# Kernel tuning notes

Measured on AMD Instinct MI355X. Metric: run time of the kernel, lower is better.

The kernel has to match this reference:

```python
import jax, jax.numpy as jnp
import numpy as np

# Model dims (match init_kwargs)
D_MODEL = 768
D_STATE = 128
HEADDIM = 64
EXPAND = 2
D_CONV = 4
D_INNER = EXPAND * D_MODEL              # 1536 (== d_ssm)
NHEADS = D_INNER // HEADDIM             # 24
CONV_DIM = D_INNER + 2 * D_STATE        # 1792
D_IN_PROJ = 2 * D_INNER + 2 * D_STATE + NHEADS  # 3352
BATCH, SEQLEN = 2, 512


def setup_inputs() -> dict:
    key = jax.random.key(0)
    ks = jax.random.split(key, 8)
    u = jax.random.normal(ks[0], (BATCH, SEQLEN, D_MODEL), jnp.float32)
    W_in = jax.random.normal(ks[1], (D_IN_PROJ, D_MODEL), jnp.float32) * 0.02
    conv_w = jax.random.normal(ks[2], (CONV_DIM, D_CONV), jnp.float32) * 0.3
    conv_b = jax.random.normal(ks[3], (CONV_DIM,), jnp.float32) * 0.1
    # dt_bias = inverse-softplus of dt sampled log-uniform in [dt_min, dt_max]
    dt = jnp.exp(jax.random.uniform(ks[4], (NHEADS,)) * (np.log(0.02) - np.log(1e-3)) + np.log(1e-3))
    dt_bias = dt + jnp.log(-jnp.expm1(-dt))
    A_log = jnp.log(jax.random.uniform(ks[5], (NHEADS,), minval=1.0, maxval=16.0))
    D_param = jnp.ones((NHEADS,), jnp.float32)
    W_out = jax.random.normal(ks[6], (D_MODEL, D_INNER), jnp.float32) * 0.02
    return dict(u=u, W_in=W_in, conv_w=conv_w, conv_b=conv_b,
                dt_bias=dt_bias, A_log=A_log, D_param=D_param, W_out=W_out)


def _mamba2_scan(u, W_in, conv_w, conv_b, dt_bias, A_log, D_param, W_out):
    B, L, _ = u.shape
    A = -jnp.exp(A_log)  # (H,)

    def step(carry, u_t):
        conv_state, ssm_state = carry  # (B, CONV_DIM, D_CONV), (B, H, P, N)
        zxbcdt = u_t @ W_in.T          # (B, D_IN_PROJ); d_mlp == 0
        z = zxbcdt[:, :D_INNER]
        xBC = zxbcdt[:, D_INNER:D_INNER + CONV_DIM]
        dt = zxbcdt[:, D_INNER + CONV_DIM:]
        # causal depthwise conv state update (roll + write last)
        conv_state = jnp.concatenate([conv_state[:, :, 1:], xBC[:, :, None]], axis=-1)
        xbc = jax.nn.silu(jnp.sum(conv_state * conv_w[None], axis=-1) + conv_b)
        x = xbc[:, :D_INNER]
        Bm = xbc[:, D_INNER:D_INNER + D_STATE]
        Cm = xbc[:, D_INNER + D_STATE:]
        dt = jax.nn.softplus(dt + dt_bias)          # (B, H)
        dA = jnp.exp(dt * A)                        # (B, H)
        xh = x.reshape(B, NHEADS, HEADDIM)          # (B, H, P)
        dBx = jnp.einsum('bh,bn,bhp->bhpn', dt, Bm, xh)
        ssm_state = ssm_state * dA[:, :, None, None] + dBx
        y = jnp.einsum('bhpn,bn->bhp', ssm_state, Cm) + D_param[None, :, None] * xh
        y = y.reshape(B, D_INNER) * jax.nn.silu(z)  # gate (rmsnorm=False)
        return (conv_state, ssm_state), y @ W_out.T

    init = (jnp.zeros((B, CONV_DIM, D_CONV), u.dtype),
            jnp.zeros((B, NHEADS, HEADDIM, D_STATE), u.dtype))
    _, ys = jax.lax.scan(jax.checkpoint(step), init, jnp.swapaxes(u, 0, 1))
    return jnp.swapaxes(ys, 0, 1)  # (B, L, D_MODEL)


def reference(u, W_in, conv_w, conv_b, dt_bias, A_log, D_param, W_out):
    return _mamba2_scan(u, W_in, conv_w, conv_b, dt_bias, A_log, D_param, W_out)
```

## Files before the change

kernel.cpp:

```cpp
#include <hip/hip_runtime.h>
#include <math.h>

#define B_     2
#define L_     512
#define DM     768
#define DS     128
#define HD     64
#define DI     1536
#define NH     24
#define CONVD  1792
#define DPROJ  3352
#define ML     (B_*L_)
#define Q      64
#define NC     (L_/Q)
#define NPAD1  3456

typedef __bf16 bf16x8 __attribute__((ext_vector_type(8)));
typedef float f32x4 __attribute__((ext_vector_type(4)));

__device__ __forceinline__ float sigmoidf_(float x){ return 1.f/(1.f+__expf(-x)); }
__device__ __forceinline__ ushort bf16rn(float x){
  uint u = __float_as_uint(x);
  u += 0x7fff + ((u>>16)&1);
  return (ushort)(u>>16);
}
__device__ __forceinline__ float bf2f(ushort h){ return __uint_as_float(((uint)h)<<16); }
__device__ __forceinline__ void gll16(const void* g, void* l){
  __builtin_amdgcn_global_load_lds((const __attribute__((address_space(1))) void*)g,
                                   (__attribute__((address_space(3))) void*)l, 16, 0, 0);
}

__device__ __forceinline__ void cvt4(const float* srcp, ushort* dsth, ushort* dstl, bool valid){
  float4 v = valid ? *(const float4*)srcp : make_float4(0,0,0,0);
  float xv[4] = {v.x,v.y,v.z,v.w};
  ushort h[4], l[4];
#pragma unroll
  for (int j=0;j<4;j++){ h[j]=bf16rn(xv[j]); l[j]=bf16rn(xv[j]-bf2f(h[j])); }
  *(uint2*)dsth = make_uint2((uint)h[0]|((uint)h[1]<<16), (uint)h[2]|((uint)h[3]<<16));
  *(uint2*)dstl = make_uint2((uint)l[0]|((uint)l[1]<<16), (uint)l[2]|((uint)l[3]<<16));
}

__launch_bounds__(256)
__global__ void cvt_all(const float* __restrict__ u, const float* __restrict__ W_in,
                        const float* __restrict__ W_out,
                        ushort* __restrict__ uS, ushort* __restrict__ WinS,
                        ushort* __restrict__ WoutS, float* __restrict__ out, int outN4){
  const int N1 = ML*(DM/4);
  const int N2 = NPAD1*(DM/4);
  const int N3 = DM*(DI/4);
  int idx = blockIdx.x*256 + threadIdx.x;
  if (idx < N1){
    int r = idx/(DM/4), c = (idx - r*(DM/4))<<2;
    cvt4(&u[(size_t)r*DM + c], &uS[(size_t)r*2*DM + c], &uS[(size_t)r*2*DM + DM + c], true);
  } else if (idx < N1+N2){
    int li = idx - N1;
    int r = li/(DM/4), c = (li - r*(DM/4))<<2;
    bool valid = r < DPROJ;
    cvt4(&W_in[(size_t)(valid ? r : 0)*DM + c], &WinS[(size_t)r*2*DM + c], &WinS[(size_t)r*2*DM + DM + c], valid);
  } else if (idx < N1+N2+N3){
    int li = idx - N1 - N2;
    int r = li/(DI/4), c = (li - r*(DI/4))<<2;
    cvt4(&W_out[(size_t)r*DI + c], &WoutS[(size_t)r*2*DI + c], &WoutS[(size_t)r*2*DI + DI + c], true);
  } else {
    int o = idx - (N1+N2+N3);
    if (o < outN4) *(float4*)&out[(size_t)o*4] = make_float4(0,0,0,0);
  }
}

template<int BM,int BN,int K,int SPLITK,bool ATOMIC>
__launch_bounds__(256, 2)
__global__ void gemm4(const ushort* __restrict__ AS, const ushort* __restrict__ BS,
                      float* __restrict__ C, int Nvalid, int Nstore){
  constexpr int KS = K / SPLITK;
  constexpr int STEPS = KS / 64;
  constexpr int WM=BM/2, WN=BN/2, FM=WM/16, FN=WN/16;
  __shared__ ushort Ah[2][BM*64], Alo[2][BM*64], Bh[2][BN*64], Blo[2][BN*64];
  const int tid=threadIdx.x, lane=tid&63, w=tid>>6;
  const int WR=w>>1, WC=w&1;
  const int bm=blockIdx.x*BM, bn=blockIdx.y*BN;
  const int kbase = blockIdx.z*KS;
  const int lr=lane&15;
  const int srow=lane>>3;
  const int scol=(((lane&7) ^ (srow&7))*8);
  f32x4 acc[FM][FN] = {};

  auto stage = [&](int d, int ks){
    int k0 = kbase + ks*64;
#pragma unroll
    for (int ci=w; ci<BM/8; ci+=4){
      size_t ro = (size_t)(bm + ci*8 + srow)*(2*K);
      gll16(&AS[ro + k0 + scol],     &Ah[d][ci*512]);
      gll16(&AS[ro + K + k0 + scol], &Alo[d][ci*512]);
    }
#pragma unroll
    for (int ci=w; ci<BN/8; ci+=4){
      size_t ro = (size_t)(bn + ci*8 + srow)*(2*K);
      gll16(&BS[ro + k0 + scol],     &Bh[d][ci*512]);
      gll16(&BS[ro + K + k0 + scol], &Blo[d][ci*512]);
    }
  };

  stage(0, 0);
  __syncthreads();
  int cur = 0;
  for (int ks=0; ks<STEPS; ks++){
    if (ks+1 < STEPS) stage(cur^1, ks+1);

    bf16x8 ah[2][FM], al[2][FM], bh[2][FN], bl[2][FN];
#pragma unroll
    for (int s2=0;s2<2;s2++){
      int gslot = s2*4 + (lane>>4);
#pragma unroll
      for (int i=0;i<FM;i++){
        int R = WR*WM + i*16 + lr;
        int so = (gslot ^ (lr&7))*8;
        ah[s2][i] = *(const bf16x8*)&Ah[cur][R*64 + so];
        al[s2][i] = *(const bf16x8*)&Alo[cur][R*64 + so];
      }
#pragma unroll
      for (int j=0;j<FN;j++){
        int R = WC*WN + j*16 + lr;
        int so = (gslot ^ (lr&7))*8;
        bh[s2][j] = *(const bf16x8*)&Bh[cur][R*64 + so];
        bl[s2][j] = *(const bf16x8*)&Blo[cur][R*64 + so];
      }
    }
#pragma unroll
    for (int s2=0;s2<2;s2++)
#pragma unroll
      for (int i=0;i<FM;i++)
#pragma unroll
        for (int j=0;j<FN;j++){
          acc[i][j] = __builtin_amdgcn_mfma_f32_16x16x32_bf16(ah[s2][i], bh[s2][j], acc[i][j], 0,0,0);
          acc[i][j] = __builtin_amdgcn_mfma_f32_16x16x32_bf16(ah[s2][i], bl[s2][j], acc[i][j], 0,0,0);
          acc[i][j] = __builtin_amdgcn_mfma_f32_16x16x32_bf16(al[s2][i], bh[s2][j], acc[i][j], 0,0,0);
        }

    __syncthreads();
    cur ^= 1;
  }

#pragma unroll
  for (int i=0;i<FM;i++)
#pragma unroll
    for (int j=0;j<FN;j++){
      int n = bn + WC*WN + j*16 + lr;
      if (n < Nvalid){
#pragma unroll
        for (int e=0;e<4;e++){
          int m = bm + WR*WM + i*16 + (lane>>4)*4 + e;
          if (ATOMIC) atomicAdd(&C[(size_t)m*Nstore + n], acc[i][j][e]);
          else        C[(size_t)m*Nstore + n] = acc[i][j][e];
        }
      }
    }
}

__launch_bounds__(256)
__global__ void conv2_kernel(const float* __restrict__ zx,
                             const float* __restrict__ cw,
                             const float* __restrict__ cb,
                             float* __restrict__ xbc){
  int g = blockIdx.x;
  int c2 = blockIdx.y;
  int b = blockIdx.z;
  int t0g = c2*32;
  int ch = g*256 + threadIdx.x;
  const float* src = zx + (size_t)(b*L_ + t0g)*DPROJ + DI + ch;
  float* dst = xbc + (size_t)(b*L_ + t0g)*CONVD + ch;
  float w0=cw[ch*4],w1=cw[ch*4+1],w2=cw[ch*4+2],w3=cw[ch*4+3],bias=cb[ch];
  float x0=0.f,x1=0.f,x2=0.f;
  if (t0g > 0){
    x0 = *(src - 3*DPROJ);
    x1 = *(src - 2*DPROJ);
    x2 = *(src - 1*DPROJ);
  }
#pragma unroll 4
  for (int tt=0; tt<32; tt++){
    float xt = src[(size_t)tt*DPROJ];
    float a = bias;
    a = fmaf(w3, xt, a); a = fmaf(w2, x2, a); a = fmaf(w1, x1, a); a = fmaf(w0, x0, a);
    dst[(size_t)tt*CONVD] = a * sigmoidf_(a);
    x0 = x1; x1 = x2; x2 = xt;
  }
}

__launch_bounds__(256)
__global__ void chunk_state_mfma(const float* __restrict__ zx,
                                 const float* __restrict__ xbc,
                                 const float* __restrict__ dt_bias,
                                 const float* __restrict__ A_log,
                                 float* __restrict__ dts, float* __restrict__ las,
                                 float* __restrict__ Schunk){
  constexpr int OX_HI=0, OX_LO=4096;
  constexpr int OB_HI=8192, OB_LO=16384;
  __shared__ ushort L[24576];
  __shared__ float Wt[64];
  int c=blockIdx.x, h=blockIdx.y, b=blockIdx.z;
  int tid=threadIdx.x;
  int bh=b*NH+h;
  const int tbase=bh*L_+c*Q;

  if (tid < 64){
    int t = c*Q + tid;
    float raw = zx[(size_t)(b*L_+t)*DPROJ + DI + CONVD + h] + dt_bias[h];
    float dtv = raw > 20.f ? raw : log1pf(__expf(raw));
    float A = -__expf(A_log[h]);
    float la = dtv*A;
#pragma unroll
    for (int off=1; off<64; off<<=1){
      float v = __shfl_up(la, off);
      if (tid >= off) la += v;
    }
    dts[tbase + tid] = dtv;
    las[tbase + tid] = la;
    float la63 = __shfl(la, 63);
    Wt[tid] = __expf(la63 - la) * dtv;
  }
  __syncthreads();

  for (int it = tid; it < 64*16; it += 256){
    int s = it >> 4, p4 = (it & 15) << 2;
    float4 v = *(const float4*)&xbc[(size_t)(b*L_ + c*Q + s)*CONVD + h*HD + p4];
    float ws = Wt[s];
    float xv[4] = {v.x*ws, v.y*ws, v.z*ws, v.w*ws};
#pragma unroll
    for (int j=0;j<4;j++){
      int p = p4 + j;
      ushort hh = bf16rn(xv[j]);
      ushort ll = bf16rn(xv[j] - bf2f(hh));
      int idx = p*64 + (((s>>3) ^ (p&7))<<3) + (s&7);
      L[OX_HI + idx] = hh; L[OX_LO + idx] = ll;
    }
  }
  for (int it = tid; it < 64*32; it += 256){
    int s = it >> 5, n4 = (it & 31) << 2;
    float4 v = *(const float4*)&xbc[(size_t)(b*L_ + c*Q + s)*CONVD + DI + n4];
    float xv[4] = {v.x,v.y,v.z,v.w};
#pragma unroll
    for (int j=0;j<4;j++){
      int n = n4 + j;
      ushort hh = bf16rn(xv[j]);
      ushort ll = bf16rn(xv[j] - bf2f(hh));
      int idx = n*64 + (((s>>3) ^ (n&7))<<3) + (s&7);
      L[OB_HI + idx] = hh; L[OB_LO + idx] = ll;
    }
  }
  __syncthreads();

  const int lane = tid & 63, w = tid >> 6;
  const int wr = w >> 1, wc = w & 1;
  const int lr = lane & 15, lk = lane >> 4;
  f32x4 acc[2][4] = {};
#pragma unroll
  for (int ks=0; ks<2; ks++){
    bf16x8 ah[2], al[2], bhf[4], blf[4];
#pragma unroll
    for (int fi=0; fi<2; fi++){
      int R = wr*32 + fi*16 + lr;
      int idx = R*64 + (((ks*4 + lk) ^ (R&7))<<3);
      ah[fi] = *(const bf16x8*)&L[OX_HI + idx];
      al[fi] = *(const bf16x8*)&L[OX_LO + idx];
    }
#pragma unroll
    for (int fj=0; fj<4; fj++){
      int Rb = wc*64 + fj*16 + lr;
      int idx = Rb*64 + (((ks*4 + lk) ^ (Rb&7))<<3);
      bhf[fj] = *(const bf16x8*)&L[OB_HI + idx];
      blf[fj] = *(const bf16x8*)&L[OB_LO + idx];
    }
#pragma unroll
    for (int fi=0; fi<2; fi++)
#pragma unroll
      for (int fj=0; fj<4; fj++){
        acc[fi][fj] = __builtin_amdgcn_mfma_f32_16x16x32_bf16(ah[fi], bhf[fj], acc[fi][fj], 0,0,0);
        acc[fi][fj] = __builtin_amdgcn_mfma_f32_16x16x32_bf16(ah[fi], blf[fj], acc[fi][fj], 0,0,0);
        acc[fi][fj] = __builtin_amdgcn_mfma_f32_16x16x32_bf16(al[fi], bhf[fj], acc[fi][fj], 0,0,0);
      }
  }

  float* Sb = Schunk + ((size_t)bh*NC + c)*(HD*DS);
#pragma unroll
  for (int fi=0; fi<2; fi++)
#pragma unroll
    for (int fj=0; fj<4; fj++){
      int n = wc*64 + fj*16 + lr;
#pragma unroll
      for (int e=0; e<4; e++){
        int p = wr*32 + fi*16 + lk*4 + e;
        Sb[p*DS + n] = acc[fi][fj][e];
      }
    }
}

__launch_bounds__(256)
__global__ void interchunk_kernel(float* __restrict__ S, const float* __restrict__ las){
  int blk = blockIdx.x;
  int slice = blk & 7; int bh = blk >> 3;
  size_t base = (size_t)bh*NC*(HD*DS) + slice*1024 + threadIdx.x*4;
  float4 run = make_float4(0,0,0,0);
#pragma unroll
  for (int c=0;c<NC;c++){
    float dec = __expf(las[bh*L_ + c*Q + 63]);
    float4 ch = *(float4*)(S + base + c*(HD*DS));
    *(float4*)(S + base + c*(HD*DS)) = run;
    run.x = fmaf(run.x, dec, ch.x);
    run.y = fmaf(run.y, dec, ch.y);
    run.z = fmaf(run.z, dec, ch.z);
    run.w = fmaf(run.w, dec, ch.w);
  }
}

__launch_bounds__(512)
__global__ void chunk_out_mfma(const float* __restrict__ zx,
                               const float* __restrict__ xbc,
                               const float* __restrict__ dts,
                               const float* __restrict__ las,
                               const float* __restrict__ Sstart,
                               const float* __restrict__ Dp,
                               ushort* __restrict__ yS){
  constexpr int OC_HI = 0,      OC_LO = 8192;
  constexpr int OP_HI = 16384,  OP_LO = 24576;
  constexpr int OX_HI = 32768,  OX_LO = 36864;
  constexpr int OG_HI = 40960,  OG_LO = 45056;
  __shared__ ushort LDSU[49152];
  __shared__ float La[64], Dt[64];

  int c = blockIdx.x, hh = blockIdx.y, b = blockIdx.z;
  int tid = threadIdx.x;
  int bh = b*NH + hh;
  const int tbase = bh*L_ + c*Q;
  const float Dh = Dp[hh];
  const int lane = tid & 63, w = tid >> 6;
  const int wr = w >> 2, wc = w & 3;
  const int lr = lane & 15, lk = lane >> 4;

  for (int it = tid; it < 64*32; it += 512){
    int t = it >> 5, n4 = (it & 31) << 2;
    float4 v = *(const float4*)&xbc[(size_t)(b*L_ + c*Q + t)*CONVD + DI + DS + n4];
    float xv[4] = {v.x,v.y,v.z,v.w};
    ushort h[4], l[4];
#pragma unroll
    for (int j=0;j<4;j++){ h[j]=bf16rn(xv[j]); l[j]=bf16rn(xv[j]-bf2f(h[j])); }
    int idx = t*128 + (((n4>>3) ^ (t&7))<<3) + (n4&7);
    *(uint2*)&LDSU[OC_HI + idx] = make_uint2((uint)h[0]|((uint)h[1]<<16), (uint)h[2]|((uint)h[3]<<16));
    *(uint2*)&LDSU[OC_LO + idx] = make_uint2((uint)l[0]|((uint)l[1]<<16), (uint)l[2]|((uint)l[3]<<16));
  }
  const float* Sb = Sstart + ((size_t)bh*NC + c)*(HD*DS);
  for (int it = tid; it < 64*32; it += 512){
    int p = it >> 5, n4 = (it & 31) << 2;
    float4 v = *(const float4*)&Sb[p*DS + n4];
    float xv[4] = {v.x,v.y,v.z,v.w};
    ushort h[4], l[4];
#pragma unroll
    for (int j=0;j<4;j++){ h[j]=bf16rn(xv[j]); l[j]=bf16rn(xv[j]-bf2f(h[j])); }
    int idx = p*128 + (((n4>>3) ^ (p&7))<<3) + (n4&7);
    *(uint2*)&LDSU[OP_HI + idx] = make_uint2((uint)h[0]|((uint)h[1]<<16), (uint)h[2]|((uint)h[3]<<16));
    *(uint2*)&LDSU[OP_LO + idx] = make_uint2((uint)l[0]|((uint)l[1]<<16), (uint)l[2]|((uint)l[3]<<16));
  }
  for (int it = tid; it < 64*16; it += 512){
    int s = it >> 4, p4 = (it & 15) << 2;
    float4 v = *(const float4*)&xbc[(size_t)(b*L_ + c*Q + s)*CONVD + hh*HD + p4];
    float xv[4] = {v.x,v.y,v.z,v.w};
#pragma unroll
    for (int j=0;j<4;j++){
      int p = p4 + j;
      ushort h = bf16rn(xv[j]);
      ushort l = bf16rn(xv[j] - bf2f(h));
      int idx = p*64 + (((s>>3) ^ (p&7))<<3) + (s&7);
      LDSU[OX_HI + idx] = h; LDSU[OX_LO + idx] = l;
    }
  }
  if (tid < 64){ La[tid] = las[tbase + tid]; Dt[tid] = dts[tbase + tid]; }
  __syncthreads();

  f32x4 yi[2] = {}, ev[2] = {}, yv[2] = {};

#pragma unroll
  for (int ks=0; ks<4; ks++){
    bf16x8 ah[2], al[2], bh, bl;
#pragma unroll
    for (int fi=0; fi<2; fi++){
      int R = wr*32 + fi*16 + lr;
      int idx = R*128 + (((ks*4 + lk) ^ (R&7))<<3);
      ah[fi] = *(const bf16x8*)&LDSU[OC_HI + idx];
      al[fi] = *(const bf16x8*)&LDSU[OC_LO + idx];
    }
    { int Rb = wc*16 + lr;
      int idx = Rb*128 + (((ks*4 + lk) ^ (Rb&7))<<3);
      bh = *(const bf16x8*)&LDSU[OP_HI + idx];
      bl = *(const bf16x8*)&LDSU[OP_LO + idx]; }
#pragma unroll
    for (int fi=0; fi<2; fi++){
      yi[fi] = __builtin_amdgcn_mfma_f32_16x16x32_bf16(ah[fi], bh, yi[fi], 0,0,0);
      yi[fi] = __builtin_amdgcn_mfma_f32_16x16x32_bf16(ah[fi], bl, yi[fi], 0,0,0);
      yi[fi] = __builtin_amdgcn_mfma_f32_16x16x32_bf16(al[fi], bh, yi[fi], 0,0,0);
    }
  }
  __syncthreads();

  for (int it = tid; it < 64*32; it += 512){
    int s = it >> 5, n4 = (it & 31) << 2;
    float4 v = *(const float4*)&xbc[(size_t)(b*L_ + c*Q + s)*CONVD + DI + n4];
    float xv[4] = {v.x,v.y,v.z,v.w};
    ushort h[4], l[4];
#pragma unroll
    for (int j=0;j<4;j++){ h[j]=bf16rn(xv[j]); l[j]=bf16rn(xv[j]-bf2f(h[j])); }
    int idx = s*128 + (((n4>>3) ^ (s&7))<<3) + (n4&7);
    *(uint2*)&LDSU[OP_HI + idx] = make_uint2((uint)h[0]|((uint)h[1]<<16), (uint)h[2]|((uint)h[3]<<16));
    *(uint2*)&LDSU[OP_LO + idx] = make_uint2((uint)l[0]|((uint)l[1]<<16), (uint)l[2]|((uint)l[3]<<16));
  }
  __syncthreads();

#pragma unroll
  for (int ks=0; ks<4; ks++){
    bf16x8 ah[2], al[2], bh, bl;
#pragma unroll
    for (int fi=0; fi<2; fi++){
      int R = wr*32 + fi*16 + lr;
      int idx = R*128 + (((ks*4 + lk) ^ (R&7))<<3);
      ah[fi] = *(const bf16x8*)&LDSU[OC_HI + idx];
      al[fi] = *(const bf16x8*)&LDSU[OC_LO + idx];
    }
    { int Rb = wc*16 + lr;
      int idx = Rb*128 + (((ks*4 + lk) ^ (Rb&7))<<3);
      bh = *(const bf16x8*)&LDSU[OP_HI + idx];
      bl = *(const bf16x8*)&LDSU[OP_LO + idx]; }
#pragma unroll
    for (int fi=0; fi<2; fi++){
      ev[fi] = __builtin_amdgcn_mfma_f32_16x16x32_bf16(ah[fi], bh, ev[fi], 0,0,0);
      ev[fi] = __builtin_amdgcn_mfma_f32_16x16x32_bf16(ah[fi], bl, ev[fi], 0,0,0);
      ev[fi] = __builtin_amdgcn_mfma_f32_16x16x32_bf16(al[fi], bh, ev[fi], 0,0,0);
    }
  }

  {
    int s_col = wc*16 + lr;
    float las_s = La[s_col], dt_s = Dt[s_col];
#pragma unroll
    for (int fi=0; fi<2; fi++)
#pragma unroll
      for (int e=0; e<4; e++){
        int t = wr*32 + fi*16 + lk*4 + e;
        float g = 0.f;
        if (s_col <= t) g = __expf(La[t] - las_s) * dt_s * ev[fi][e];
        ushort hg = bf16rn(g);
        ushort lg = bf16rn(g - bf2f(hg));
        int idx = t*64 + (((s_col>>3) ^ (t&7))<<3) + (s_col&7);
        LDSU[OG_HI + idx] = hg; LDSU[OG_LO + idx] = lg;
      }
  }
  __syncthreads();

#pragma unroll
  for (int ks=0; ks<2; ks++){
    bf16x8 ah[2], al[2], bh, bl;
#pragma unroll
    for (int fi=0; fi<2; fi++){
      int R = wr*32 + fi*16 + lr;
      int idx = R*64 + (((ks*4 + lk) ^ (R&7))<<3);
      ah[fi] = *(const bf16x8*)&LDSU[OG_HI + idx];
      al[fi] = *(const bf16x8*)&LDSU[OG_LO + idx];
    }
    { int Rb = wc*16 + lr;
      int idx = Rb*64 + (((ks*4 + lk) ^ (Rb&7))<<3);
      bh = *(const bf16x8*)&LDSU[OX_HI + idx];
      bl = *(const bf16x8*)&LDSU[OX_LO + idx]; }
#pragma unroll
    for (int fi=0; fi<2; fi++){
      yv[fi] = __builtin_amdgcn_mfma_f32_16x16x32_bf16(ah[fi], bh, yv[fi], 0,0,0);
      yv[fi] = __builtin_amdgcn_mfma_f32_16x16x32_bf16(ah[fi], bl, yv[fi], 0,0,0);
      yv[fi] = __builtin_amdgcn_mfma_f32_16x16x32_bf16(al[fi], bh, yv[fi], 0,0,0);
    }
  }
  __syncthreads();

  {
    float* Yf = (float*)&LDSU[OG_HI];
    int p = wc*16 + lr;
#pragma unroll
    for (int fi=0; fi<2; fi++)
#pragma unroll
      for (int e=0; e<4; e++){
        int t = wr*32 + fi*16 + lk*4 + e;
        Yf[t*64 + p] = __expf(La[t])*yi[fi][e] + yv[fi][e];
      }
  }
  __syncthreads();

  {
    const float* Yf = (const float*)&LDSU[OG_HI];
    for (int it = tid; it < 64*16; it += 512){
      int t = it >> 4, p4 = (it & 15) << 2;
      size_t row = (size_t)(b*L_ + c*Q + t);
      float4 x4 = *(const float4*)&xbc[row*CONVD + hh*HD + p4];
      float4 z4 = *(const float4*)&zx[row*DPROJ + hh*HD + p4];
      float xx[4] = {x4.x,x4.y,x4.z,x4.w};
      float zz[4] = {z4.x,z4.y,z4.z,z4.w};
      ushort h4[4], l4[4];
#pragma unroll
      for (int j=0;j<4;j++){
        float y = Yf[t*64 + p4 + j] + Dh*xx[j];
        float o = y * (zz[j] * sigmoidf_(zz[j]));
        h4[j] = bf16rn(o);
        l4[j] = bf16rn(o - bf2f(h4[j]));
      }
      size_t o0 = row*(size_t)(2*DI) + hh*HD + p4;
      *(uint2*)&yS[o0]      = make_uint2((uint)h4[0]|((uint)h4[1]<<16), (uint)h4[2]|((uint)h4[3]<<16));
      *(uint2*)&yS[o0 + DI] = make_uint2((uint)l4[0]|((uint)l4[1]<<16), (uint)l4[2]|((uint)l4[3]<<16));
    }
  }
}

extern "C" void kernel_launch(void* const* d_in, const int* in_sizes, int n_in,
                              void* d_out, int out_size, void* d_ws, size_t ws_size,
                              hipStream_t stream) {
  const float* u       = (const float*)d_in[0];
  const float* W_in    = (const float*)d_in[1];
  const float* conv_w  = (const float*)d_in[2];
  const float* conv_b  = (const float*)d_in[3];
  const float* dt_bias = (const float*)d_in[4];
  const float* A_log   = (const float*)d_in[5];
  const float* D_param = (const float*)d_in[6];
  const float* W_out   = (const float*)d_in[7];
  float* out = (float*)d_out;

  float* ws = (float*)d_ws;
  float* zx     = ws;
  float* xbc    = zx   + (size_t)ML*DPROJ;
  float* dts    = xbc  + (size_t)ML*CONVD;
  float* las    = dts  + (size_t)B_*NH*L_;
  float* Schunk = las  + (size_t)B_*NH*L_;
  ushort* uS    = (ushort*)(Schunk + (size_t)B_*NH*NC*HD*DS);
  ushort* yS    = uS;
  ushort* WinS  = uS + (size_t)ML*2*DI;
  ushort* WoutS = WinS + (size_t)NPAD1*2*DM;

  {
    int outN4 = out_size/4;
    int total = ML*(DM/4) + NPAD1*(DM/4) + DM*(DI/4) + outN4;
    cvt_all<<<(total+255)/256, 256, 0, stream>>>(u, W_in, W_out, uS, WinS, WoutS, out, outN4);
  }
  {
    dim3 grid(ML/64, NPAD1/64, 1);
    gemm4<64,64,DM,1,false><<<grid, 256, 0, stream>>>(uS, WinS, zx, DPROJ, DPROJ);
  }
  {
    dim3 grid(7, L_/32, B_);
    conv2_kernel<<<grid, 256, 0, stream>>>(zx, conv_w, conv_b, xbc);
  }
  {
    dim3 grid(NC, NH, B_);
    chunk_state_mfma<<<grid, 256, 0, stream>>>(zx, xbc, dt_bias, A_log, dts, las, Schunk);
  }
  interchunk_kernel<<<B_*NH*8, 256, 0, stream>>>(Schunk, las);
  {
    dim3 grid(NC, NH, B_);
    chunk_out_mfma<<<grid, 512, 0, stream>>>(zx, xbc, dts, las, Schunk, D_param, yS);
  }
  {
    dim3 grid(ML/64, DM/64, 4);
    gemm4<64,64,DI,4,true><<<grid, 256, 0, stream>>>(yS, WoutS, out, DM, DM);
  }
}
```

Before: 175.3 us.

## Replace split-bf16 three-pass GEMMs with single-pass fp16 MFMA and compute dt separately

Both projection GEMMs now use a single fp16 MFMA per tile instead of three bf16 hi/lo MFMAs. This cuts GEMM compute, LDS use and operand memory roughly threefold. The dt columns of the input projection are split out into a dedicated fp32 dot-product path inside the conversion kernel, so the main GEMM width becomes 3328, a multiple of 64, and needs no padding. The cost is lower precision: fp16 keeps about 11 mantissa bits where the hi/lo split emulated near-fp32, and values risk overflow or loss of small magnitudes.

```diff
diff --git a/kernel.cpp b/kernel.cpp
--- a/kernel.cpp
+++ b/kernel.cpp
@@ -9,13 +9,13 @@
 #define DI     1536
 #define NH     24
 #define CONVD  1792
-#define DPROJ  3352
+#define ZROW   3328
 #define ML     (B_*L_)
 #define Q      64
 #define NC     (L_/Q)
-#define NPAD1  3456
 
 typedef __bf16 bf16x8 __attribute__((ext_vector_type(8)));
+typedef _Float16 h16x8 __attribute__((ext_vector_type(8)));
 typedef float f32x4 __attribute__((ext_vector_type(4)));
 
 __device__ __forceinline__ float sigmoidf_(float x){ return 1.f/(1.f+__expf(-x)); }
@@ -25,56 +25,70 @@
   return (ushort)(u>>16);
 }
 __device__ __forceinline__ float bf2f(ushort h){ return __uint_as_float(((uint)h)<<16); }
+__device__ __forceinline__ ushort f16rn(float x){
+  _Float16 h = (_Float16)x;
+  union { _Float16 f; ushort u; } cv; cv.f = h; return cv.u;
+}
 __device__ __forceinline__ void gll16(const void* g, void* l){
   __builtin_amdgcn_global_load_lds((const __attribute__((address_space(1))) void*)g,
                                    (__attribute__((address_space(3))) void*)l, 16, 0, 0);
 }
 
-__device__ __forceinline__ void cvt4(const float* srcp, ushort* dsth, ushort* dstl, bool valid){
-  float4 v = valid ? *(const float4*)srcp : make_float4(0,0,0,0);
-  float xv[4] = {v.x,v.y,v.z,v.w};
-  ushort h[4], l[4];
-#pragma unroll
-  for (int j=0;j<4;j++){ h[j]=bf16rn(xv[j]); l[j]=bf16rn(xv[j]-bf2f(h[j])); }
-  *(uint2*)dsth = make_uint2((uint)h[0]|((uint)h[1]<<16), (uint)h[2]|((uint)h[3]<<16));
-  *(uint2*)dstl = make_uint2((uint)l[0]|((uint)l[1]<<16), (uint)l[2]|((uint)l[3]<<16));
-}
-
 __launch_bounds__(256)
 __global__ void cvt_all(const float* __restrict__ u, const float* __restrict__ W_in,
                         const float* __restrict__ W_out,
-                        ushort* __restrict__ uS, ushort* __restrict__ WinS,
-                        ushort* __restrict__ WoutS, float* __restrict__ out, int outN4){
+                        ushort* __restrict__ uH, ushort* __restrict__ WinH,
+                        ushort* __restrict__ WoutH, float* __restrict__ dtraw,
+                        float* __restrict__ out, int outN4){
   const int N1 = ML*(DM/4);
-  const int N2 = NPAD1*(DM/4);
+  const int N2 = ZROW*(DM/4);
   const int N3 = DM*(DI/4);
+  const int N4 = ML*NH;
   int idx = blockIdx.x*256 + threadIdx.x;
   if (idx < N1){
     int r = idx/(DM/4), c = (idx - r*(DM/4))<<2;
-    cvt4(&u[(size_t)r*DM + c], &uS[(size_t)r*2*DM + c], &uS[(size_t)r*2*DM + DM + c], true);
+    float4 v = *(const float4*)&u[(size_t)r*DM + c];
+    ushort h[4] = {f16rn(v.x), f16rn(v.y), f16rn(v.z), f16rn(v.w)};
+    *(uint2*)&uH[(size_t)r*DM + c] = make_uint2((uint)h[0]|((uint)h[1]<<16), (uint)h[2]|((uint)h[3]<<16));
   } else if (idx < N1+N2){
     int li = idx - N1;
     int r = li/(DM/4), c = (li - r*(DM/4))<<2;
-    bool valid = r < DPROJ;
-    cvt4(&W_in[(size_t)(valid ? r : 0)*DM + c], &WinS[(size_t)r*2*DM + c], &WinS[(size_t)r*2*DM + DM + c], valid);
+    float4 v = *(const float4*)&W_in[(size_t)r*DM + c];
+    ushort h[4] = {f16rn(v.x), f16rn(v.y), f16rn(v.z), f16rn(v.w)};
+    *(uint2*)&WinH[(size_t)r*DM + c] = make_uint2((uint)h[0]|((uint)h[1]<<16), (uint)h[2]|((uint)h[3]<<16));
   } else if (idx < N1+N2+N3){
     int li = idx - N1 - N2;
     int r = li/(DI/4), c = (li - r*(DI/4))<<2;
-    cvt4(&W_out[(size_t)r*DI + c], &WoutS[(size_t)r*2*DI + c], &WoutS[(size_t)r*2*DI + DI + c], true);
+    float4 v = *(const float4*)&W_out[(size_t)r*DI + c];
+    ushort h[4] = {f16rn(v.x), f16rn(v.y), f16rn(v.z), f16rn(v.w)};
+    *(uint2*)&WoutH[(size_t)r*DI + c] = make_uint2((uint)h[0]|((uint)h[1]<<16), (uint)h[2]|((uint)h[3]<<16));
+  } else if (idx < N1+N2+N3+N4){
+    int li = idx - (N1+N2+N3);
+    int m = li/NH, h = li - (li/NH)*NH;
+    const float* ur = u + (size_t)m*DM;
+    const float* wr = W_in + (size_t)(ZROW + h)*DM;
+    float acc = 0.f;
+#pragma unroll 4
+    for (int k=0; k<DM; k+=4){
+      float4 a = *(const float4*)&ur[k];
+      float4 b = *(const float4*)&wr[k];
+      acc = fmaf(a.x,b.x, fmaf(a.y,b.y, fmaf(a.z,b.z, fmaf(a.w,b.w, acc))));
+    }
+    dtraw[(size_t)m*NH + h] = acc;
   } else {
-    int o = idx - (N1+N2+N3);
+    int o = idx - (N1+N2+N3+N4);
     if (o < outN4) *(float4*)&out[(size_t)o*4] = make_float4(0,0,0,0);
   }
 }
 
 template<int BM,int BN,int K,int SPLITK,bool ATOMIC>
 __launch_bounds__(256, 2)
-__global__ void gemm4(const ushort* __restrict__ AS, const ushort* __restrict__ BS,
-                      float* __restrict__ C, int Nvalid, int Nstore){
+__global__ void gemm_f16(const ushort* __restrict__ AS, const ushort* __restrict__ BS,
+                         float* __restrict__ C, int Nvalid, int Nstore){
   constexpr int KS = K / SPLITK;
   constexpr int STEPS = KS / 64;
   constexpr int WM=BM/2, WN=BN/2, FM=WM/16, FN=WN/16;
-  __shared__ ushort Ah[2][BM*64], Alo[2][BM*64], Bh[2][BN*64], Blo[2][BN*64];
+  __shared__ ushort Ah[2][BM*64], Bh[2][BN*64];
   const int tid=threadIdx.x, lane=tid&63, w=tid>>6;
   const int WR=w>>1, WC=w&1;
   const int bm=blockIdx.x*BM, bn=blockIdx.y*BN;
@@ -87,17 +101,11 @@
   auto stage = [&](int d, int ks){
     int k0 = kbase + ks*64;
 #pragma unroll
-    for (int ci=w; ci<BM/8; ci+=4){
-      size_t ro = (size_t)(bm + ci*8 + srow)*(2*K);
-      gll16(&AS[ro + k0 + scol],     &Ah[d][ci*512]);
-      gll16(&AS[ro + K + k0 + scol], &Alo[d][ci*512]);
-    }
-#pragma unroll
-    for (int ci=w; ci<BN/8; ci+=4){
-      size_t ro = (size_t)(bn + ci*8 + srow)*(2*K);
-      gll16(&BS[ro + k0 + scol],     &Bh[d][ci*512]);
-      gll16(&BS[ro + K + k0 + scol], &Blo[d][ci*512]);
-    }
+    for (int ci=w; ci<BM/8; ci+=4)
+      gll16(&AS[(size_t)(bm + ci*8 + srow)*K + k0 + scol], &Ah[d][ci*512]);
+#pragma unroll
+    for (int ci=w; ci<BN/8; ci+=4)
+      gll16(&BS[(size_t)(bn + ci*8 + srow)*K + k0 + scol], &Bh[d][ci*512]);
   };
 
   stage(0, 0);
@@ -106,23 +114,19 @@
   for (int ks=0; ks<STEPS; ks++){
     if (ks+1 < STEPS) stage(cur^1, ks+1);
 
-    bf16x8 ah[2][FM], al[2][FM], bh[2][FN], bl[2][FN];
+    h16x8 af[2][FM], bf[2][FN];
 #pragma unroll
     for (int s2=0;s2<2;s2++){
       int gslot = s2*4 + (lane>>4);
 #pragma unroll
       for (int i=0;i<FM;i++){
         int R = WR*WM + i*16 + lr;
-        int so = (gslot ^ (lr&7))*8;
-        ah[s2][i] = *(const bf16x8*)&Ah[cur][R*64 + so];
-        al[s2][i] = *(const bf16x8*)&Alo[cur][R*64 + so];
+        af[s2][i] = *(const h16x8*)&Ah[cur][R*64 + (gslot ^ (lr&7))*8];
       }
 #pragma unroll
       for (int j=0;j<FN;j++){
         int R = WC*WN + j*16 + lr;
-        int so = (gslot ^ (lr&7))*8;
-        bh[s2][j] = *(const bf16x8*)&Bh[cur][R*64 + so];
-        bl[s2][j] = *(const bf16x8*)&Blo[cur][R*64 + so];
+        bf[s2][j] = *(const h16x8*)&Bh[cur][R*64 + (gslot ^ (lr&7))*8];
       }
     }
 #pragma unroll
@@ -130,11 +134,8 @@
 #pragma unroll
       for (int i=0;i<FM;i++)
 #pragma unroll
-        for (int j=0;j<FN;j++){
-          acc[i][j] = __builtin_amdgcn_mfma_f32_16x16x32_bf16(ah[s2][i], bh[s2][j], acc[i][j], 0,0,0);
-          acc[i][j] = __builtin_amdgcn_mfma_f32_16x16x32_bf16(ah[s2][i], bl[s2][j], acc[i][j], 0,0,0);
-          acc[i][j] = __builtin_amdgcn_mfma_f32_16x16x32_bf16(al[s2][i], bh[s2][j], acc[i][j], 0,0,0);
-        }
+        for (int j=0;j<FN;j++)
+          acc[i][j] = __builtin_amdgcn_mfma_f32_16x16x32_f16(af[s2][i], bf[s2][j], acc[i][j], 0,0,0);
 
     __syncthreads();
     cur ^= 1;
@@ -166,18 +167,18 @@
   int b = blockIdx.z;
   int t0g = c2*32;
   int ch = g*256 + threadIdx.x;
-  const float* src = zx + (size_t)(b*L_ + t0g)*DPROJ + DI + ch;
+  const float* src = zx + (size_t)(b*L_ + t0g)*ZROW + DI + ch;
   float* dst = xbc + (size_t)(b*L_ + t0g)*CONVD + ch;
   float w0=cw[ch*4],w1=cw[ch*4+1],w2=cw[ch*4+2],w3=cw[ch*4+3],bias=cb[ch];
   float x0=0.f,x1=0.f,x2=0.f;
   if (t0g > 0){
-    x0 = *(src - 3*DPROJ);
-    x1 = *(src - 2*DPROJ);
-    x2 = *(src - 1*DPROJ);
+    x0 = *(src - 3*ZROW);
+    x1 = *(src - 2*ZROW);
+    x2 = *(src - 1*ZROW);
   }
 #pragma unroll 4
   for (int tt=0; tt<32; tt++){
-    float xt = src[(size_t)tt*DPROJ];
+    float xt = src[(size_t)tt*ZROW];
     float a = bias;
     a = fmaf(w3, xt, a); a = fmaf(w2, x2, a); a = fmaf(w1, x1, a); a = fmaf(w0, x0, a);
     dst[(size_t)tt*CONVD] = a * sigmoidf_(a);
@@ -186,7 +187,7 @@
 }
 
 __launch_bounds__(256)
-__global__ void chunk_state_mfma(const float* __restrict__ zx,
+__global__ void chunk_state_mfma(const float* __restrict__ dtraw,
                                  const float* __restrict__ xbc,
                                  const float* __restrict__ dt_bias,
                                  const float* __restrict__ A_log,
@@ -203,7 +204,7 @@
 
   if (tid < 64){
     int t = c*Q + tid;
-    float raw = zx[(size_t)(b*L_+t)*DPROJ + DI + CONVD + h] + dt_bias[h];
+    float raw = dtraw[(size_t)(b*L_+t)*NH + h] + dt_bias[h];
     float dtv = raw > 20.f ? raw : log1pf(__expf(raw));
     float A = -__expf(A_log[h]);
     float la = dtv*A;
@@ -494,20 +495,18 @@
       int t = it >> 4, p4 = (it & 15) << 2;
       size_t row = (size_t)(b*L_ + c*Q + t);
       float4 x4 = *(const float4*)&xbc[row*CONVD + hh*HD + p4];
-      float4 z4 = *(const float4*)&zx[row*DPROJ + hh*HD + p4];
+      float4 z4 = *(const float4*)&zx[row*ZROW + hh*HD + p4];
       float xx[4] = {x4.x,x4.y,x4.z,x4.w};
       float zz[4] = {z4.x,z4.y,z4.z,z4.w};
-      ushort h4[4], l4[4];
+      ushort h4[4];
 #pragma unroll
       for (int j=0;j<4;j++){
         float y = Yf[t*64 + p4 + j] + Dh*xx[j];
         float o = y * (zz[j] * sigmoidf_(zz[j]));
-        h4[j] = bf16rn(o);
-        l4[j] = bf16rn(o - bf2f(h4[j]));
-      }
-      size_t o0 = row*(size_t)(2*DI) + hh*HD + p4;
-      *(uint2*)&yS[o0]      = make_uint2((uint)h4[0]|((uint)h4[1]<<16), (uint)h4[2]|((uint)h4[3]<<16));
-      *(uint2*)&yS[o0 + DI] = make_uint2((uint)l4[0]|((uint)l4[1]<<16), (uint)l4[2]|((uint)l4[3]<<16));
+        h4[j] = f16rn(o);
+      }
+      size_t o0 = row*(size_t)DI + hh*HD + p4;
+      *(uint2*)&yS[o0] = make_uint2((uint)h4[0]|((uint)h4[1]<<16), (uint)h4[2]|((uint)h4[3]<<16));
     }
   }
 }
@@ -527,23 +526,24 @@
 
   float* ws = (float*)d_ws;
   float* zx     = ws;
-  float* xbc    = zx   + (size_t)ML*DPROJ;
+  float* xbc    = zx   + (size_t)ML*ZROW;
   float* dts    = xbc  + (size_t)ML*CONVD;
   float* las    = dts  + (size_t)B_*NH*L_;
-  float* Schunk = las  + (size_t)B_*NH*L_;
-  ushort* uS    = (ushort*)(Schunk + (size_t)B_*NH*NC*HD*DS);
-  ushort* yS    = uS;
-  ushort* WinS  = uS + (size_t)ML*2*DI;
-  ushort* WoutS = WinS + (size_t)NPAD1*2*DM;
+  float* dtraw  = las  + (size_t)B_*NH*L_;
+  float* Schunk = dtraw + (size_t)ML*NH;
+  ushort* uH    = (ushort*)(Schunk + (size_t)B_*NH*NC*HD*DS);
+  ushort* yS    = uH;
+  ushort* WinH  = uH + (size_t)ML*DI;
+  ushort* WoutH = WinH + (size_t)ZROW*DM;
 
   {
     int outN4 = out_size/4;
-    int total = ML*(DM/4) + NPAD1*(DM/4) + DM*(DI/4) + outN4;
-    cvt_all<<<(total+255)/256, 256, 0, stream>>>(u, W_in, W_out, uS, WinS, WoutS, out, outN4);
-  }
-  {
-    dim3 grid(ML/64, NPAD1/64, 1);
-    gemm4<64,64,DM,1,false><<<grid, 256, 0, stream>>>(uS, WinS, zx, DPROJ, DPROJ);
+    int total = ML*(DM/4) + ZROW*(DM/4) + DM*(DI/4) + ML*NH + outN4;
+    cvt_all<<<(total+255)/256, 256, 0, stream>>>(u, W_in, W_out, uH, WinH, WoutH, dtraw, out, outN4);
+  }
+  {
+    dim3 grid(ML/64, ZROW/64, 1);
+    gemm_f16<64,64,DM,1,false><<<grid, 256, 0, stream>>>(uH, WinH, zx, ZROW, ZROW);
   }
   {
     dim3 grid(7, L_/32, B_);
@@ -551,7 +551,7 @@
   }
   {
     dim3 grid(NC, NH, B_);
-    chunk_state_mfma<<<grid, 256, 0, stream>>>(zx, xbc, dt_bias, A_log, dts, las, Schunk);
+    chunk_state_mfma<<<grid, 256, 0, stream>>>(dtraw, xbc, dt_bias, A_log, dts, las, Schunk);
   }
   interchunk_kernel<<<B_*NH*8, 256, 0, stream>>>(Schunk, las);
   {
@@ -560,6 +560,6 @@
   }
   {
     dim3 grid(ML/64, DM/64, 4);
-    gemm4<64,64,DI,4,true><<<grid, 256, 0, stream>>>(yS, WoutS, out, DM, DM);
-  }
-}
+    gemm_f16<64,64,DI,4,true><<<grid, 256, 0, stream>>>(yS, WoutH, out, DM, DM);
+  }
+}
```

Result: slower. 233.5 us (+33.2%).
